# Kernel tuning notes

Measured on AMD Instinct MI355X. Metric: run time of the kernel, lower is better.

The kernel has to match this reference:

```python
import jax, jax.numpy as jnp
import numpy as np

B, S, D, H = 2, 2048, 1024, 16
DH = D // H  # head dim = 64


def _split_heads(x):
    # [B,S,D] -> [B,H,S,DH]
    return x.reshape(B, S, H, DH).transpose(0, 2, 1, 3)


def setup_inputs() -> dict:
    key = jax.random.key(0)
    ks = jax.random.split(key, 14)
    sc = 1.0 / np.sqrt(D)
    p = {"hidden_states": jax.random.normal(ks[0], (B, S, D), jnp.float32)}
    names = ["Wq", "Wk1", "Wk2", "Wv1", "Wv2", "Wd"]
    for i, n in enumerate(names):
        p[n] = jax.random.normal(ks[1 + 2 * i], (D, D), jnp.float32) * sc
        p["b" + n[1:]] = jax.random.normal(ks[2 + 2 * i], (D,), jnp.float32) * 0.02
    return p


def reference(hidden_states, Wq, bq, Wk1, bk1, Wk2, bk2, Wv1, bv1, Wv2, bv2, Wd, bd):
    q = _split_heads(hidden_states @ Wq + bq)
    k1 = _split_heads(hidden_states @ Wk1 + bk1)
    k2 = _split_heads(hidden_states @ Wk2 + bk2)
    v1 = _split_heads(hidden_states @ Wv1 + bv1)
    v2 = _split_heads(hidden_states @ Wv2 + bv2)

    scores = jnp.einsum("bhqd,bhkd->bhqk", q, k1) / np.sqrt(DH)
    causal = jnp.tril(jnp.ones((S, S), dtype=bool))  # True = keep
    scores = jnp.where(causal, scores, -jnp.inf)
    probs = jax.nn.softmax(scores, axis=-1)

    ctx = jnp.einsum("bhqk,bhkd->bhqd", probs, v1)          # [B,H,S,DH]
    ctx = jnp.einsum("bhqd,bhkd->bhqk", ctx, k2)            # [B,H,S,S]
    ctx = jnp.einsum("bhqk,bhkd->bhqd", ctx, v2)            # [B,H,S,DH]

    ctx = ctx.transpose(0, 2, 1, 3).reshape(B, S, D)
    return ctx @ Wd + bd
```

## Files before the change

kernel.cpp:

```cpp
#include <hip/hip_runtime.h>
#include <hip/hip_bf16.h>

typedef __bf16 bf16x8 __attribute__((ext_vector_type(8)));
typedef float f32x4 __attribute__((ext_vector_type(4)));
using bf16 = __hip_bfloat16;

#define SEQ 2048
#define DM 1024
#define NH 16
#define DH 64
#define NBH 32
#define MR 4096

#define WAITBAR(N) asm volatile("s_waitcnt vmcnt(" #N ")\n\ts_barrier" ::: "memory")

static __device__ __forceinline__ void async_cp16(const void* gsrc, void* ldsdst) {
  __builtin_amdgcn_global_load_lds((__attribute__((address_space(1))) void*)gsrc,
                                   (__attribute__((address_space(3))) void*)ldsdst, 16, 0, 0);
}

static __device__ __forceinline__ unsigned short f2bfu(float f) {
  bf16 h = __float2bfloat16(f);
  unsigned short u; __builtin_memcpy(&u, &h, 2); return u;
}
static __device__ __forceinline__ unsigned int pack_bf2(float lo, float hi) {
  return (unsigned int)f2bfu(lo) | ((unsigned int)f2bfu(hi) << 16);
}

__global__ __launch_bounds__(256) void cast_x(const float* __restrict__ X, bf16* __restrict__ Xb) {
  long g = ((long)blockIdx.x * 256 + threadIdx.x) * 8;
  float4 a = *(const float4*)(X + g);
  float4 b = *(const float4*)(X + g + 4);
  unsigned short u[8];
  u[0]=f2bfu(a.x); u[1]=f2bfu(a.y); u[2]=f2bfu(a.z); u[3]=f2bfu(a.w);
  u[4]=f2bfu(b.x); u[5]=f2bfu(b.y); u[6]=f2bfu(b.z); u[7]=f2bfu(b.w);
  uint4 o; __builtin_memcpy(&o, u, 16);
  *(uint4*)(Xb + g) = o;
}

struct WPtrs { const float* w[6]; };

__global__ __launch_bounds__(256) void transpose_cast_w(WPtrs wp, bf16* __restrict__ WtAll) {
  const int z = blockIdx.z;
  const float* W = wp.w[z];
  bf16* Wt = WtAll + (long)z * DM * DM;
  __shared__ float Ts[32][33];
  int n0 = blockIdx.x * 32, k0 = blockIdx.y * 32;
  int tx = threadIdx.x, ty = threadIdx.y;
#pragma unroll
  for (int it = 0; it < 4; ++it)
    Ts[ty + 8*it][tx] = W[(long)(k0 + ty + 8*it) * DM + n0 + tx];
  __syncthreads();
#pragma unroll
  for (int it = 0; it < 4; ++it)
    Wt[(long)(n0 + ty + 8*it) * DM + k0 + tx] = __float2bfloat16(Ts[tx][ty + 8*it]);
}

struct ProjArgs {
  const float* bias[5];
  bf16* out[5];
};

__global__ __launch_bounds__(256, 2) void gemm_proj(const bf16* __restrict__ A,
                                                    const bf16* __restrict__ WtAll, ProjArgs p) {
  __shared__ alignas(16) bf16 SM[36864];
  bf16* As = SM;
  bf16* Bs = SM + 12288;
  const int tid = threadIdx.x;
  const int bid = blockIdx.x;
  const int wave = tid >> 6, lane = tid & 63, l15 = lane & 15, l4 = lane >> 4;
  const int wm = wave >> 1, wn = wave & 1;
  const int slot8 = (l4 ^ ((l15 >> 1) & 3)) * 8;
  const int prow = tid >> 2;
  const int cc = (tid & 3) ^ ((prow >> 1) & 3);
  char* dA = (char*)As + wave * 1024;
  char* dB = (char*)Bs + wave * 1024;

  if (bid < 512) {
    const int mt = bid & 31, nt = bid >> 5;
    const int m0 = mt * 128;
    const int z = nt >> 2;
    const int n0z = (nt & 3) * 256;
    const bf16* Bt = WtAll + (long)z * DM * DM + (long)n0z * DM;

    const bf16* sA0 = A  + (long)(m0 + prow) * DM + cc * 8;
    const bf16* sA1 = sA0 + 64L * DM;
    const bf16* sB0 = Bt + (long)prow * DM + cc * 8;
    const bf16* sB1 = sB0 + 64L * DM;
    const bf16* sB2 = sB0 + 128L * DM;
    const bf16* sB3 = sB0 + 192L * DM;

#define PSTAGE(KT_, BUF_) do {                                  \
    int ko_ = (KT_) * 32;                                       \
    async_cp16(sA0 + ko_, dA + (BUF_) * 8192);                  \
    async_cp16(sA1 + ko_, dA + (BUF_) * 8192 + 4096);           \
    async_cp16(sB0 + ko_, dB + (BUF_) * 16384);                 \
    async_cp16(sB1 + ko_, dB + (BUF_) * 16384 + 4096);          \
    async_cp16(sB2 + ko_, dB + (BUF_) * 16384 + 8192);          \
    async_cp16(sB3 + ko_, dB + (BUF_) * 16384 + 12288);         \
  } while (0)

    const int arow = wm * 64 + l15;
    const int brow = wn * 128 + l15;
    f32x4 acc[4][8] = {};

#define PCOMPUTE(BUF_) do {                                                        \
    const bf16* ab_ = As + (BUF_) * 4096;                                          \
    const bf16* bb_ = Bs + (BUF_) * 8192;                                          \
    bf16x8 af_[4], bq_[8];                                                         \
    _Pragma("unroll")                                                              \
    for (int i = 0; i < 4; ++i) af_[i] = *(const bf16x8*)(ab_ + (arow + i * 16) * 32 + slot8); \
    _Pragma("unroll")                                                              \
    for (int j = 0; j < 8; ++j) bq_[j] = *(const bf16x8*)(bb_ + (brow + j * 16) * 32 + slot8); \
    _Pragma("unroll")                                                              \
    for (int i = 0; i < 4; ++i)                                                    \
      _Pragma("unroll")                                                            \
      for (int j = 0; j < 8; ++j)                                                  \
        acc[i][j] = __builtin_amdgcn_mfma_f32_16x16x32_bf16(af_[i], bq_[j], acc[i][j], 0, 0, 0); \
  } while (0)

    PSTAGE(0, 0);
    PSTAGE(1, 1);
    int buf = 0;
#pragma unroll 1
    for (int k = 0; k < 31; ++k) {
      WAITBAR(6);
      if (k < 30) {
        int nb = buf + 2; if (nb > 2) nb -= 3;
        PSTAGE(k + 2, nb);
      }
      PCOMPUTE(buf);
      ++buf; if (buf > 2) buf = 0;
    }
    WAITBAR(0);
    PCOMPUTE(buf);
#undef PSTAGE
#undef PCOMPUTE

    const float* bias = p.bias[z];
    bf16* out = p.out[z];
    float bv[8];
#pragma unroll
    for (int j = 0; j < 8; ++j) bv[j] = bias[n0z + wn * 128 + j * 16 + l15];

    if (z < 2) {
      const float scale = (z == 0) ? 0.125f * 1.44269504f : 1.0f;
#pragma unroll
      for (int i = 0; i < 4; ++i)
#pragma unroll
        for (int j = 0; j < 8; ++j)
#pragma unroll
          for (int r = 0; r < 4; ++r) {
            int m = m0 + wm * 64 + i * 16 + l4 * 4 + r;
            int n = n0z + wn * 128 + j * 16 + l15;
            int b = m >> 11, s = m & 2047, hh = n >> 6, d = n & 63;
            out[((long)((b * NH + hh) * SEQ + s)) * DH + d] =
                __float2bfloat16((acc[i][j][r] + bv[j]) * scale);
          }
    } else {
      __syncthreads();
      bf16* Os = SM;
#pragma unroll
      for (int i = 0; i < 4; ++i)
#pragma unroll
        for (int j = 0; j < 8; ++j)
#pragma unroll
          for (int r = 0; r < 4; ++r) {
            int nl = wn * 128 + j * 16 + l15;
            int ml = wm * 64 + i * 16 + l4 * 4 + r;
            Os[nl * 136 + ml] = __float2bfloat16(acc[i][j][r] + bv[j]);
          }
      __syncthreads();
      {
        int nl = tid;
        int ng = n0z + nl;
        int hh = ng >> 6, d = ng & 63;
        int b = m0 >> 11, s0 = m0 & 2047;
        bf16* op = out + ((long)((b * NH + hh) * DH + d)) * SEQ + s0;
#pragma unroll
        for (int u = 0; u < 16; ++u)
          *(bf16x8*)(op + u * 8) = *(const bf16x8*)(Os + nl * 136 + u * 8);
      }
    }
  } else {
    const int tb = bid - 512;
    const int mt = tb & 31, nt16 = tb >> 5;
    const int m0 = mt * 128, n0 = nt16 * 64;
    const bf16* Bt = WtAll + 4L * DM * DM + (long)n0 * DM;

    const bf16* sA0 = A + (long)(m0 + prow) * DM + cc * 8;
    const bf16* sA1 = sA0 + 64L * DM;
    const bf16* sB0 = Bt + (long)prow * DM + cc * 8;

#define TSTAGE(KT_, BUF_) do {                                  \
    int ko_ = (KT_) * 32;                                       \
    async_cp16(sA0 + ko_, dA + (BUF_) * 8192);                  \
    async_cp16(sA1 + ko_, dA + (BUF_) * 8192 + 4096);           \
    async_cp16(sB0 + ko_, dB + (BUF_) * 4096);                  \
  } while (0)

    const int arow = wm * 64 + l15;
    const int brow = wn * 32 + l15;
    f32x4 acc2[4][2] = {};

#define TCOMPUTE(BUF_) do {                                                        \
    const bf16* ab_ = As + (BUF_) * 4096;                                          \
    const bf16* bb_ = Bs + (BUF_) * 2048;                                          \
    bf16x8 af_[4], bq_[2];                                                         \
    _Pragma("unroll")                                                              \
    for (int i = 0; i < 4; ++i) af_[i] = *(const bf16x8*)(ab_ + (arow + i * 16) * 32 + slot8); \
    _Pragma("unroll")                                                              \
    for (int j = 0; j < 2; ++j) bq_[j] = *(const bf16x8*)(bb_ + (brow + j * 16) * 32 + slot8); \
    _Pragma("unroll")                                                              \
    for (int i = 0; i < 4; ++i)                                                    \
      _Pragma("unroll")                                                            \
      for (int j = 0; j < 2; ++j)                                                  \
        acc2[i][j] = __builtin_amdgcn_mfma_f32_16x16x32_bf16(af_[i], bq_[j], acc2[i][j], 0, 0, 0); \
  } while (0)

    TSTAGE(0, 0);
    TSTAGE(1, 1);
    int buf = 0;
#pragma unroll 1
    for (int k = 0; k < 31; ++k) {
      WAITBAR(3);
      if (k < 30) {
        int nb = buf + 2; if (nb > 2) nb -= 3;
        TSTAGE(k + 2, nb);
      }
      TCOMPUTE(buf);
      ++buf; if (buf > 2) buf = 0;
    }
    WAITBAR(0);
    TCOMPUTE(buf);
#undef TSTAGE
#undef TCOMPUTE

    float bv2[2];
#pragma unroll
    for (int j = 0; j < 2; ++j) bv2[j] = p.bias[4][n0 + wn * 32 + j * 16 + l15];
    __syncthreads();
    bf16* Os = SM;
#pragma unroll
    for (int i = 0; i < 4; ++i)
#pragma unroll
      for (int j = 0; j < 2; ++j)
#pragma unroll
        for (int r = 0; r < 4; ++r) {
          int nl = wn * 32 + j * 16 + l15;
          int ml = wm * 64 + i * 16 + l4 * 4 + r;
          Os[nl * 136 + ml] = __float2bfloat16(acc2[i][j][r] + bv2[j]);
        }
    __syncthreads();
    {
      int nl = tid & 63, seg = tid >> 6;
      int ng = n0 + nl;
      int hh = ng >> 6, d = ng & 63;
      int b = m0 >> 11, s0 = m0 & 2047;
      bf16* op = p.out[4] + ((long)((b * NH + hh) * DH + d)) * SEQ + s0 + seg * 32;
#pragma unroll
      for (int u = 0; u < 4; ++u)
        *(bf16x8*)(op + u * 8) = *(const bf16x8*)(Os + nl * 136 + seg * 32 + u * 8);
    }
  }
}

static __device__ __forceinline__ void gemm_core128(
    const bf16* __restrict__ A, const bf16* __restrict__ Bt,
    bf16* As, bf16* Bs, f32x4 (&acc)[4][4], int m0, int tid)
{
  const int wave = tid >> 6, lane = tid & 63, l15 = lane & 15, l4 = lane >> 4;
  const int wm = wave >> 1, wn = wave & 1;
  const int r0 = tid >> 2;
  const int c0 = (tid & 3) ^ ((r0 >> 1) & 3);
  const bf16* srcA0 = A + (long)(m0 + r0) * DM + c0 * 8;
  const bf16* srcA1 = A + (long)(m0 + r0 + 64) * DM + c0 * 8;
  const bf16* srcB0 = Bt + (long)r0 * DM + c0 * 8;
  const bf16* srcB1 = Bt + (long)(r0 + 64) * DM + c0 * 8;
  char* dstA = (char*)As + wave * 1024;
  char* dstB = (char*)Bs + wave * 1024;

#define STAGE(KT_, BUF_) do {                                   \
    int ko_ = (KT_) * 32;                                       \
    int bo_ = (BUF_) * 8192;                                    \
    async_cp16(srcA0 + ko_, dstA + bo_);                        \
    async_cp16(srcA1 + ko_, dstA + bo_ + 4096);                 \
    async_cp16(srcB0 + ko_, dstB + bo_);                        \
    async_cp16(srcB1 + ko_, dstB + bo_ + 4096);                 \
  } while (0)

  const int slot8 = (l4 ^ ((l15 >> 1) & 3)) * 8;
  const int arow = wm * 64 + l15;
  const int brow = wn * 64 + l15;

#define COMPUTE(BUF_) do {                                                         \
    const bf16* ab_ = As + (BUF_) * 4096;                                          \
    const bf16* bb_ = Bs + (BUF_) * 4096;                                          \
    bf16x8 af_[4], bq_[4];                                                         \
    _Pragma("unroll")                                                              \
    for (int i = 0; i < 4; ++i) af_[i] = *(const bf16x8*)(ab_ + (arow + i * 16) * 32 + slot8); \
    _Pragma("unroll")                                                              \
    for (int j = 0; j < 4; ++j) bq_[j] = *(const bf16x8*)(bb_ + (brow + j * 16) * 32 + slot8); \
    _Pragma("unroll")                                                              \
    for (int i = 0; i < 4; ++i)                                                    \
      _Pragma("unroll")                                                            \
      for (int j = 0; j < 4; ++j)                                                  \
        acc[i][j] = __builtin_amdgcn_mfma_f32_16x16x32_bf16(af_[i], bq_[j], acc[i][j], 0, 0, 0); \
  } while (0)

  STAGE(0, 0);
  STAGE(1, 1);
  int buf = 0;
#pragma unroll 1
  for (int k = 0; k < 31; ++k) {
    WAITBAR(4);
    if (k < 30) {
      int nb = buf + 2; if (nb > 2) nb -= 3;
      STAGE(k + 2, nb);
    }
    COMPUTE(buf);
    ++buf; if (buf > 2) buf = 0;
  }
  WAITBAR(0);
  COMPUTE(buf);
#undef STAGE
#undef COMPUTE
}

__global__ __launch_bounds__(256, 3) void gemm_out(const bf16* __restrict__ A, const bf16* __restrict__ Bt,
                                                   const float* __restrict__ bias, float* __restrict__ out) {
  __shared__ alignas(16) bf16 As[3 * 128 * 32];
  __shared__ alignas(16) bf16 Bs[3 * 128 * 32];
  const int tid = threadIdx.x;
  const int bid = blockIdx.x;
  const int nt = bid & 7, mt = bid >> 3;
  const int m0 = mt * 128, n0 = nt * 128;
  f32x4 acc[4][4] = {};
  gemm_core128(A, Bt + (long)n0 * DM, As, Bs, acc, m0, tid);
  const int wave = tid >> 6, lane = tid & 63, l15 = lane & 15, l4 = lane >> 4;
  const int wm = wave >> 1, wn = wave & 1;
  float bv[4];
#pragma unroll
  for (int j = 0; j < 4; ++j) bv[j] = bias[n0 + wn * 64 + j * 16 + l15];
#pragma unroll
  for (int i = 0; i < 4; ++i)
#pragma unroll
    for (int j = 0; j < 4; ++j)
#pragma unroll
      for (int r = 0; r < 4; ++r) {
        int m = m0 + wm * 64 + i * 16 + l4 * 4 + r;
        int n = n0 + wn * 64 + j * 16 + l15;
        out[(long)m * DM + n] = acc[i][j][r] + bv[j];
      }
}

__global__ __launch_bounds__(256) void m_kernel(
    const bf16* __restrict__ k2t, const bf16* __restrict__ v2t, float* __restrict__ Mbuf)
{
  const int scx = blockIdx.x;
  const int bh = blockIdx.y;
  const int tid = threadIdx.x, wave = tid >> 6, lane = tid & 63, l15 = lane & 15, l4 = lane >> 4;
  const bf16* kp = k2t + (long)bh * DH * SEQ;
  const bf16* vp = v2t + (long)bh * DH * SEQ;
  __shared__ alignas(16) bf16 K2s[64 * 32];
  __shared__ alignas(16) bf16 V2s[64 * 32];
  f32x4 acc[4] = {};
  const int s0 = scx * 256;
  for (int kk = 0; kk < 256; kk += 32) {
    __syncthreads();
    {
      int c = tid, r = c >> 2, pp = c & 3;
      async_cp16(kp + (long)r * SEQ + s0 + kk + pp * 8, K2s + wave * 64 * 8);
      async_cp16(vp + (long)r * SEQ + s0 + kk + pp * 8, V2s + wave * 64 * 8);
    }
    __syncthreads();
    int arow = 16 * wave + l15;
    bf16x8 a = *(const bf16x8*)(K2s + arow * 32 + l4 * 8);
#pragma unroll
    for (int nb = 0; nb < 4; ++nb) {
      int col = nb * 16 + l15;
      bf16x8 b = *(const bf16x8*)(V2s + col * 32 + l4 * 8);
      acc[nb] = __builtin_amdgcn_mfma_f32_16x16x32_bf16(a, b, acc[nb], 0, 0, 0);
    }
  }
  float* Mp = Mbuf + (long)bh * 4096;
#pragma unroll
  for (int nb = 0; nb < 4; ++nb)
#pragma unroll
    for (int r = 0; r < 4; ++r) {
      int row = 16 * wave + l4 * 4 + r;
      int col = nb * 16 + l15;
      atomicAdd(Mp + row * 64 + col, acc[nb][r]);
    }
}

static __device__ __forceinline__ void redist(const unsigned int (&pk)[4][2], bf16x8 (&pb)[2],
                                              int l4, int l15) {
#pragma unroll
  for (int h = 0; h < 2; ++h) {
    unsigned int w4[4];
#pragma unroll
    for (int w = 0; w < 4; ++w) {
      int src = l15 + 16 * (2 * (l4 & 1) + (w >> 1));
      unsigned int va = (unsigned int)__shfl((int)pk[2 * h][w & 1], src);
      unsigned int vb = (unsigned int)__shfl((int)pk[2 * h + 1][w & 1], src);
      w4[w] = (l4 & 2) ? vb : va;
    }
    __builtin_memcpy(&pb[h], w4, 16);
  }
}

__global__ __launch_bounds__(256) void attn_fused(
    const bf16* __restrict__ q,
    const bf16* __restrict__ k1,
    const bf16* __restrict__ v1t,
    const float* __restrict__ Mbuf,
    bf16* __restrict__ ctx2)
{
  const int bid = blockIdx.x;
  const int xcd = bid & 7, ii = bid >> 3;
  const int bh = (xcd << 2) | (ii & 3);
  const int qpair = ii >> 2;
  const int bb = bh >> 4, hh = bh & 15;
  const int tid = threadIdx.x, wave = tid >> 6, lane = tid & 63;
  const int l15 = lane & 15, l4 = lane >> 4;
  const bf16* qp = q   + (long)bh * SEQ * DH;
  const bf16* kp = k1  + (long)bh * SEQ * DH;
  const bf16* vp = v1t + (long)bh * DH * SEQ;
  const float* Mp = Mbuf + (long)bh * 4096;

  __shared__ alignas(16) bf16 Ks[2][128 * 64];
  __shared__ alignas(16) bf16 Vs[2][64 * 128];

  bf16x8 mf[4][2];
#pragma unroll
  for (int db = 0; db < 4; ++db)
#pragma unroll
    for (int h = 0; h < 2; ++h) {
      bf16x8 t;
#pragma unroll
      for (int j = 0; j < 8; ++j)
        t[j] = (__bf16)Mp[(32 * h + 8 * l4 + j) * 64 + 16 * db + l15];
      mf[db][h] = t;
    }

#define STAGE_KV(JJ, BUF) do {                                                     \
    int kv0_ = 128 * (JJ);                                                         \
    int cK_ = (tid & 7) ^ ((tid >> 3) & 7);                                        \
    int cV_ = (tid & 15) ^ ((tid >> 4) & 15);                                      \
    _Pragma("unroll")                                                              \
    for (int p_ = 0; p_ < 4; ++p_) {                                               \
      int rK_ = (tid >> 3) + 32 * p_;                                              \
      async_cp16(kp + (long)(kv0_ + rK_) * DH + cK_ * 8,                           \
                 (char*)Ks[BUF] + p_ * 4096 + wave * 1024);                        \
      int rV_ = (tid >> 4) + 16 * p_;                                              \
      async_cp16(vp + (long)rV_ * SEQ + kv0_ + cV_ * 8,                            \
                 (char*)Vs[BUF] + p_ * 4096 + wave * 1024);                        \
    }                                                                              \
  } while (0)

#pragma unroll 1
  for (int half = 0; half < 2; ++half) {
    const int tq = (half == 0) ? (31 - qpair) : qpair;
    const int Q0 = 64 * tq;
    const int qg = Q0 + 16 * wave + l15;
    const int jm = tq >> 1;

    __syncthreads();
    STAGE_KV(0, 0);

    bf16x8 aq[2];
#pragma unroll
    for (int h = 0; h < 2; ++h)
      aq[h] = *(const bf16x8*)(qp + (long)qg * DH + 32 * h + 8 * l4);

    float m_run = -__builtin_inff(), l_run = 0.f;
    f32x4 acc_o[4] = {};

    __syncthreads();

#pragma unroll 1
    for (int j = 0; j <= jm; ++j) {
      const int cur = j & 1;
      if (j < jm) STAGE_KV(j + 1, cur ^ 1);

      f32x4 sc[8] = {};
#pragma unroll
      for (int nb = 0; nb < 8; ++nb) {
        const bf16* krow = Ks[cur] + (16 * nb + l15) * 64;
#pragma unroll
        for (int h = 0; h < 2; ++h) {
          bf16x8 kf = *(const bf16x8*)(krow + (((4 * h + l4) ^ (l15 & 7)) * 8));
          sc[nb] = __builtin_amdgcn_mfma_f32_16x16x32_bf16(kf, aq[h], sc[nb], 0, 0, 0);
        }
      }

      if (j == jm) {
        const int kv0 = 128 * j;
#pragma unroll
        for (int nb = 0; nb < 8; ++nb)
#pragma unroll
          for (int r = 0; r < 4; ++r)
            if (kv0 + 16 * nb + 4 * l4 + r > qg) sc[nb][r] = -__builtin_inff();
      }

      float tmax = -__builtin_inff();
#pragma unroll
      for (int nb = 0; nb < 8; ++nb)
#pragma unroll
        for (int r = 0; r < 4; ++r) tmax = fmaxf(tmax, sc[nb][r]);
      tmax = fmaxf(tmax, __shfl_xor(tmax, 16));
      tmax = fmaxf(tmax, __shfl_xor(tmax, 32));
      float mnew = fmaxf(m_run, tmax);
      float sf = __builtin_amdgcn_exp2f(m_run - mnew);
      m_run = mnew;

      float ssum = 0.f;
      unsigned int pkA[4][2], pkB[4][2];
#pragma unroll
      for (int nb = 0; nb < 4; ++nb)
#pragma unroll
        for (int pr = 0; pr < 2; ++pr) {
          float p0 = __builtin_amdgcn_exp2f(sc[nb][2 * pr]     - mnew);
          float p1 = __builtin_amdgcn_exp2f(sc[nb][2 * pr + 1] - mnew);
          ssum += p0 + p1;
          pkA[nb][pr] = pack_bf2(p0, p1);
        }
#pragma unroll
      for (int nb = 0; nb < 4; ++nb)
#pragma unroll
        for (int pr = 0; pr < 2; ++pr) {
          float p0 = __builtin_amdgcn_exp2f(sc[nb + 4][2 * pr]     - mnew);
          float p1 = __builtin_amdgcn_exp2f(sc[nb + 4][2 * pr + 1] - mnew);
          ssum += p0 + p1;
          pkB[nb][pr] = pack_bf2(p0, p1);
        }
      ssum += __shfl_xor(ssum, 16);
      ssum += __shfl_xor(ssum, 32);
      l_run = l_run * sf + ssum;
#pragma unroll
      for (int db = 0; db < 4; ++db)
#pragma unroll
        for (int r = 0; r < 4; ++r) acc_o[db][r] *= sf;

      bf16x8 pbA[2], pbB[2];
      redist(pkA, pbA, l4, l15);
      redist(pkB, pbB, l4, l15);
#pragma unroll
      for (int db = 0; db < 4; ++db) {
        const bf16* vrow = Vs[cur] + (16 * db + l15) * 128;
#pragma unroll
        for (int hs = 0; hs < 2; ++hs) {
          bf16x8 vf = *(const bf16x8*)(vrow + (((4 * hs + l4) ^ l15) * 8));
          acc_o[db] = __builtin_amdgcn_mfma_f32_16x16x32_bf16(vf, pbA[hs], acc_o[db], 0, 0, 0);
        }
#pragma unroll
        for (int hs = 0; hs < 2; ++hs) {
          bf16x8 vf = *(const bf16x8*)(vrow + (((4 * (hs + 2) + l4) ^ l15) * 8));
          acc_o[db] = __builtin_amdgcn_mfma_f32_16x16x32_bf16(vf, pbB[hs], acc_o[db], 0, 0, 0);
        }
      }
      __syncthreads();
    }

    float invl = __builtin_amdgcn_rcpf(l_run);
    unsigned int ck[4][2];
#pragma unroll
    for (int db = 0; db < 4; ++db)
#pragma unroll
      for (int pr = 0; pr < 2; ++pr)
        ck[db][pr] = pack_bf2(acc_o[db][2 * pr] * invl, acc_o[db][2 * pr + 1] * invl);
    bf16x8 cb[2];
    redist(ck, cb, l4, l15);
    f32x4 o2[4] = {};
#pragma unroll
    for (int db = 0; db < 4; ++db)
#pragma unroll
      for (int h = 0; h < 2; ++h)
        o2[db] = __builtin_amdgcn_mfma_f32_16x16x32_bf16(mf[db][h], cb[h], o2[db], 0, 0, 0);

    bf16* Os = (bf16*)Ks;
#pragma unroll
    for (int db = 0; db < 4; ++db)
#pragma unroll
      for (int r = 0; r < 4; ++r)
        Os[(16 * wave + l15) * 72 + 16 * db + 4 * l4 + r] = __float2bfloat16(o2[db][r]);
    __syncthreads();
    {
      int rr = tid >> 2, cc2 = tid & 3;
      long obase = ((long)(bb * SEQ + Q0 + rr)) * DM + hh * DH + cc2 * 16;
      *(bf16x8*)(ctx2 + obase)     = *(const bf16x8*)(Os + rr * 72 + cc2 * 16);
      *(bf16x8*)(ctx2 + obase + 8) = *(const bf16x8*)(Os + rr * 72 + cc2 * 16 + 8);
    }
  }
#undef STAGE_KV
}

extern "C" void kernel_launch(void* const* d_in, const int* in_sizes, int n_in,
                              void* d_out, int out_size, void* d_ws, size_t ws_size,
                              hipStream_t stream) {
  (void)in_sizes; (void)n_in; (void)out_size; (void)ws_size;
  const float* X = (const float*)d_in[0];
  const float* W[6]    = {(const float*)d_in[1], (const float*)d_in[3], (const float*)d_in[5],
                          (const float*)d_in[7], (const float*)d_in[9], (const float*)d_in[11]};
  const float* bias[6] = {(const float*)d_in[2], (const float*)d_in[4], (const float*)d_in[6],
                          (const float*)d_in[8], (const float*)d_in[10], (const float*)d_in[12]};

  char* ws = (char*)d_ws;
  bf16* Xb  = (bf16*)(ws);
  bf16* Wt  = (bf16*)(ws + (8L  << 20));
  bf16* qB  = (bf16*)(ws + (20L << 20));
  bf16* k1B = (bf16*)(ws + (28L << 20));
  bf16* k2t = (bf16*)(ws + (36L << 20));
  bf16* v1t = (bf16*)(ws + (44L << 20));
  bf16* v2t = (bf16*)(ws + (52L << 20));
  float* Mb = (float*)(ws + (60L << 20));
  bf16* c2  = Xb;

  cast_x<<<2048, 256, 0, stream>>>(X, Xb);

  WPtrs wp; for (int z = 0; z < 6; ++z) wp.w[z] = W[z];
  transpose_cast_w<<<dim3(32, 32, 6), dim3(32, 8), 0, stream>>>(wp, Wt);

  ProjArgs pa;
  for (int z = 0; z < 5; ++z) pa.bias[z] = bias[z];
  pa.out[0] = qB; pa.out[1] = k1B; pa.out[2] = k2t; pa.out[3] = v1t; pa.out[4] = v2t;
  gemm_proj<<<1024, 256, 0, stream>>>(Xb, Wt, pa);

  hipMemsetAsync(Mb, 0, (size_t)NBH * 4096 * 4, stream);
  m_kernel<<<dim3(8, 32), 256, 0, stream>>>(k2t, v2t, Mb);

  attn_fused<<<512, 256, 0, stream>>>(qB, k1B, v1t, Mb, c2);

  gemm_out<<<256, 256, 0, stream>>>(c2, Wt + 5L * DM * DM, bias[5], (float*)d_out);
}
```

Before: 152.2 us.

## Narrow output GEMM tile, add MFMA priority hints and lazy softmax rescale

The output projection GEMM now uses 128x64 tiles instead of 128x128, doubling the grid from 256 to 512 blocks so more of the GPU's compute units get work. In the fused attention kernel, s_setprio raises wave priority around the MFMA blocks, and the running-max rescale of the accumulator and row sum is skipped when no lane's max increased. These changes target under-filled compute units and redundant exp and multiply work. The trade-off is more redundant A-tile loads in the GEMM and an extra wave-wide vote branch in the attention inner loop.

```diff
diff --git a/kernel.cpp b/kernel.cpp
--- a/kernel.cpp
+++ b/kernel.cpp
@@ -265,92 +265,81 @@
   }
 }
 
-static __device__ __forceinline__ void gemm_core128(
-    const bf16* __restrict__ A, const bf16* __restrict__ Bt,
-    bf16* As, bf16* Bs, f32x4 (&acc)[4][4], int m0, int tid)
-{
+__global__ __launch_bounds__(256, 3) void gemm_out(const bf16* __restrict__ A, const bf16* __restrict__ Bt,
+                                                   const float* __restrict__ bias, float* __restrict__ out) {
+  __shared__ alignas(16) bf16 As[3 * 128 * 32];
+  __shared__ alignas(16) bf16 Bs[3 * 64 * 32];
+  const int tid = threadIdx.x;
+  const int bid = blockIdx.x;
+  const int nt = bid & 15, mt = bid >> 4;
+  const int m0 = mt * 128, n0 = nt * 64;
   const int wave = tid >> 6, lane = tid & 63, l15 = lane & 15, l4 = lane >> 4;
   const int wm = wave >> 1, wn = wave & 1;
-  const int r0 = tid >> 2;
-  const int c0 = (tid & 3) ^ ((r0 >> 1) & 3);
-  const bf16* srcA0 = A + (long)(m0 + r0) * DM + c0 * 8;
-  const bf16* srcA1 = A + (long)(m0 + r0 + 64) * DM + c0 * 8;
-  const bf16* srcB0 = Bt + (long)r0 * DM + c0 * 8;
-  const bf16* srcB1 = Bt + (long)(r0 + 64) * DM + c0 * 8;
-  char* dstA = (char*)As + wave * 1024;
-  char* dstB = (char*)Bs + wave * 1024;
-
-#define STAGE(KT_, BUF_) do {                                   \
+  const int slot8 = (l4 ^ ((l15 >> 1) & 3)) * 8;
+  const int prow = tid >> 2;
+  const int cc = (tid & 3) ^ ((prow >> 1) & 3);
+  const bf16* sA0 = A + (long)(m0 + prow) * DM + cc * 8;
+  const bf16* sA1 = sA0 + 64L * DM;
+  const bf16* sB0 = Bt + (long)(n0 + prow) * DM + cc * 8;
+  char* dA = (char*)As + wave * 1024;
+  char* dB = (char*)Bs + wave * 1024;
+
+#define OSTAGE(KT_, BUF_) do {                                  \
     int ko_ = (KT_) * 32;                                       \
-    int bo_ = (BUF_) * 8192;                                    \
-    async_cp16(srcA0 + ko_, dstA + bo_);                        \
-    async_cp16(srcA1 + ko_, dstA + bo_ + 4096);                 \
-    async_cp16(srcB0 + ko_, dstB + bo_);                        \
-    async_cp16(srcB1 + ko_, dstB + bo_ + 4096);                 \
+    async_cp16(sA0 + ko_, dA + (BUF_) * 8192);                  \
+    async_cp16(sA1 + ko_, dA + (BUF_) * 8192 + 4096);           \
+    async_cp16(sB0 + ko_, dB + (BUF_) * 4096);                  \
   } while (0)
 
-  const int slot8 = (l4 ^ ((l15 >> 1) & 3)) * 8;
   const int arow = wm * 64 + l15;
-  const int brow = wn * 64 + l15;
-
-#define COMPUTE(BUF_) do {                                                         \
+  const int brow = wn * 32 + l15;
+  f32x4 acc2[4][2] = {};
+
+#define OCOMPUTE(BUF_) do {                                                        \
     const bf16* ab_ = As + (BUF_) * 4096;                                          \
-    const bf16* bb_ = Bs + (BUF_) * 4096;                                          \
-    bf16x8 af_[4], bq_[4];                                                         \
+    const bf16* bb_ = Bs + (BUF_) * 2048;                                          \
+    bf16x8 af_[4], bq_[2];                                                         \
     _Pragma("unroll")                                                              \
     for (int i = 0; i < 4; ++i) af_[i] = *(const bf16x8*)(ab_ + (arow + i * 16) * 32 + slot8); \
     _Pragma("unroll")                                                              \
-    for (int j = 0; j < 4; ++j) bq_[j] = *(const bf16x8*)(bb_ + (brow + j * 16) * 32 + slot8); \
+    for (int j = 0; j < 2; ++j) bq_[j] = *(const bf16x8*)(bb_ + (brow + j * 16) * 32 + slot8); \
     _Pragma("unroll")                                                              \
     for (int i = 0; i < 4; ++i)                                                    \
       _Pragma("unroll")                                                            \
-      for (int j = 0; j < 4; ++j)                                                  \
-        acc[i][j] = __builtin_amdgcn_mfma_f32_16x16x32_bf16(af_[i], bq_[j], acc[i][j], 0, 0, 0); \
+      for (int j = 0; j < 2; ++j)                                                  \
+        acc2[i][j] = __builtin_amdgcn_mfma_f32_16x16x32_bf16(af_[i], bq_[j], acc2[i][j], 0, 0, 0); \
   } while (0)
 
-  STAGE(0, 0);
-  STAGE(1, 1);
+  OSTAGE(0, 0);
+  OSTAGE(1, 1);
   int buf = 0;
 #pragma unroll 1
   for (int k = 0; k < 31; ++k) {
-    WAITBAR(4);
+    WAITBAR(3);
     if (k < 30) {
       int nb = buf + 2; if (nb > 2) nb -= 3;
-      STAGE(k + 2, nb);
-    }
-    COMPUTE(buf);
+      OSTAGE(k + 2, nb);
+    }
+    OCOMPUTE(buf);
     ++buf; if (buf > 2) buf = 0;
   }
   WAITBAR(0);
-  COMPUTE(buf);
-#undef STAGE
-#undef COMPUTE
-}
-
-__global__ __launch_bounds__(256, 3) void gemm_out(const bf16* __restrict__ A, const bf16* __restrict__ Bt,
-                                                   const float* __restrict__ bias, float* __restrict__ out) {
-  __shared__ alignas(16) bf16 As[3 * 128 * 32];
-  __shared__ alignas(16) bf16 Bs[3 * 128 * 32];
-  const int tid = threadIdx.x;
-  const int bid = blockIdx.x;
-  const int nt = bid & 7, mt = bid >> 3;
-  const int m0 = mt * 128, n0 = nt * 128;
-  f32x4 acc[4][4] = {};
-  gemm_core128(A, Bt + (long)n0 * DM, As, Bs, acc, m0, tid);
-  const int wave = tid >> 6, lane = tid & 63, l15 = lane & 15, l4 = lane >> 4;
-  const int wm = wave >> 1, wn = wave & 1;
-  float bv[4];
-#pragma unroll
-  for (int j = 0; j < 4; ++j) bv[j] = bias[n0 + wn * 64 + j * 16 + l15];
+  OCOMPUTE(buf);
+#undef OSTAGE
+#undef OCOMPUTE
+
+  float bv[2];
+#pragma unroll
+  for (int j = 0; j < 2; ++j) bv[j] = bias[n0 + wn * 32 + j * 16 + l15];
 #pragma unroll
   for (int i = 0; i < 4; ++i)
 #pragma unroll
-    for (int j = 0; j < 4; ++j)
+    for (int j = 0; j < 2; ++j)
 #pragma unroll
       for (int r = 0; r < 4; ++r) {
         int m = m0 + wm * 64 + i * 16 + l4 * 4 + r;
-        int n = n0 + wn * 64 + j * 16 + l15;
-        out[(long)m * DM + n] = acc[i][j][r] + bv[j];
+        int n = n0 + wn * 32 + j * 16 + l15;
+        out[(long)m * DM + n] = acc2[i][j][r] + bv[j];
       }
 }
 
@@ -485,6 +474,7 @@
       if (j < jm) STAGE_KV(j + 1, cur ^ 1);
 
       f32x4 sc[8] = {};
+      __builtin_amdgcn_s_setprio(1);
 #pragma unroll
       for (int nb = 0; nb < 8; ++nb) {
         const bf16* krow = Ks[cur] + (16 * nb + l15) * 64;
@@ -494,6 +484,7 @@
           sc[nb] = __builtin_amdgcn_mfma_f32_16x16x32_bf16(kf, aq[h], sc[nb], 0, 0, 0);
         }
       }
+      __builtin_amdgcn_s_setprio(0);
 
       if (j == jm) {
         const int kv0 = 128 * j;
@@ -511,9 +502,17 @@
         for (int r = 0; r < 4; ++r) tmax = fmaxf(tmax, sc[nb][r]);
       tmax = fmaxf(tmax, __shfl_xor(tmax, 16));
       tmax = fmaxf(tmax, __shfl_xor(tmax, 32));
-      float mnew = fmaxf(m_run, tmax);
-      float sf = __builtin_amdgcn_exp2f(m_run - mnew);
-      m_run = mnew;
+
+      if (!__all(tmax <= m_run)) {
+        float mnew = fmaxf(m_run, tmax);
+        float sf = __builtin_amdgcn_exp2f(m_run - mnew);
+        m_run = mnew;
+        l_run *= sf;
+#pragma unroll
+        for (int db = 0; db < 4; ++db)
+#pragma unroll
+          for (int r = 0; r < 4; ++r) acc_o[db][r] *= sf;
+      }
 
       float ssum = 0.f;
       unsigned int pkA[4][2], pkB[4][2];
@@ -521,8 +520,8 @@
       for (int nb = 0; nb < 4; ++nb)
 #pragma unroll
         for (int pr = 0; pr < 2; ++pr) {
-          float p0 = __builtin_amdgcn_exp2f(sc[nb][2 * pr]     - mnew);
-          float p1 = __builtin_amdgcn_exp2f(sc[nb][2 * pr + 1] - mnew);
+          float p0 = __builtin_amdgcn_exp2f(sc[nb][2 * pr]     - m_run);
+          float p1 = __builtin_amdgcn_exp2f(sc[nb][2 * pr + 1] - m_run);
           ssum += p0 + p1;
           pkA[nb][pr] = pack_bf2(p0, p1);
         }
@@ -530,22 +529,19 @@
       for (int nb = 0; nb < 4; ++nb)
 #pragma unroll
         for (int pr = 0; pr < 2; ++pr) {
-          float p0 = __builtin_amdgcn_exp2f(sc[nb + 4][2 * pr]     - mnew);
-          float p1 = __builtin_amdgcn_exp2f(sc[nb + 4][2 * pr + 1] - mnew);
+          float p0 = __builtin_amdgcn_exp2f(sc[nb + 4][2 * pr]     - m_run);
+          float p1 = __builtin_amdgcn_exp2f(sc[nb + 4][2 * pr + 1] - m_run);
           ssum += p0 + p1;
           pkB[nb][pr] = pack_bf2(p0, p1);
         }
       ssum += __shfl_xor(ssum, 16);
       ssum += __shfl_xor(ssum, 32);
-      l_run = l_run * sf + ssum;
-#pragma unroll
-      for (int db = 0; db < 4; ++db)
-#pragma unroll
-        for (int r = 0; r < 4; ++r) acc_o[db][r] *= sf;
+      l_run += ssum;
 
       bf16x8 pbA[2], pbB[2];
       redist(pkA, pbA, l4, l15);
       redist(pkB, pbB, l4, l15);
+      __builtin_amdgcn_s_setprio(1);
 #pragma unroll
       for (int db = 0; db < 4; ++db) {
         const bf16* vrow = Vs[cur] + (16 * db + l15) * 128;
@@ -560,6 +556,7 @@
           acc_o[db] = __builtin_amdgcn_mfma_f32_16x16x32_bf16(vf, pbB[hs], acc_o[db], 0, 0, 0);
         }
       }
+      __builtin_amdgcn_s_setprio(0);
       __syncthreads();
     }
 
@@ -632,5 +629,5 @@
 
   attn_fused<<<512, 256, 0, stream>>>(qB, k1B, v1t, Mb, c2);
 
-  gemm_out<<<256, 256, 0, stream>>>(c2, Wt + 5L * DM * DM, bias[5], (float*)d_out);
-}
+  gemm_out<<<512, 256, 0, stream>>>(c2, Wt + 5L * DM * DM, bias[5], (float*)d_out);
+}
```

Result: faster. 146.4 us, median of 3 (-3.8%).
